# Optimization experiments

Hardware: AMD Instinct MI355X
Metric: run time of the kernel (lower is better)

The kernel has to match this reference:

```python
import jax, jax.numpy as jnp
import numpy as np

B, IN, K, E = 2048, 1024, 128, 64  # batch, in_features, n_concepts, emb_size


def setup_inputs() -> dict:
    key = jax.random.key(0)
    k1, k2, k3, k4, k5 = jax.random.split(key, 5)
    x = jax.random.normal(k1, (B, IN), dtype=jnp.float32)
    # stacked per-concept Linear(in_features, 2*emb_size)
    W = jax.random.normal(k2, (K, IN, 2 * E), dtype=jnp.float32) * (1.0 / np.sqrt(IN))
    b = jax.random.normal(k3, (K, 2 * E), dtype=jnp.float32) * 0.01
    # shared prob predictor Linear(2*emb_size, 1)
    wp = jax.random.normal(k4, (2 * E,), dtype=jnp.float32) * (1.0 / np.sqrt(2 * E))
    bp = jax.random.normal(k5, (), dtype=jnp.float32) * 0.01
    return {"x": x, "W": W, "b": b, "wp": wp, "bp": bp}


def reference(x, W, b, wp, bp):
    # batched GEMM over all concepts at once: [B,K,2E]
    context = jax.nn.leaky_relu(jnp.einsum('bi,kio->bko', x, W) + b)
    # shared predictor + sigmoid: [B,K]
    c_pred = jax.nn.sigmoid(jnp.einsum('bko,o->bk', context, wp) + bp)
    ctx_pos = context[..., :E]
    ctx_neg = context[..., E:]
    p = c_pred[..., None]
    c_emb = ctx_pos * p + ctx_neg * (1.0 - p)  # [B,K,E]
    return c_emb, c_pred
```

## Files before the change

### kernel.cpp

```cpp
#include <hip/hip_runtime.h>

typedef unsigned int u32;
typedef unsigned short u16;
typedef __attribute__((ext_vector_type(8))) __bf16 bf16x8;
typedef __attribute__((ext_vector_type(4))) float f32x4;

#define B_SZ 2048
#define IN_SZ 1024
#define K_SZ 128
#define E_SZ 64
#define TWOE 128
static const size_t OUT_EMB = (size_t)B_SZ * K_SZ * E_SZ;

__device__ __forceinline__ u16 f2bf(float f) {
    u32 u = __builtin_bit_cast(u32, f);
    u32 r = u + 0x7fffu + ((u >> 16) & 1u);
    return (u16)(r >> 16);
}

__device__ __forceinline__ void async16(const void* g, void* l) {
    __builtin_amdgcn_global_load_lds((const __attribute__((address_space(1))) u32*)g,
                                     (__attribute__((address_space(3))) u32*)l, 16, 0, 0);
}

__global__ void __launch_bounds__(256) cvt_x(const float* __restrict__ in, u16* __restrict__ outp, int n4) {
    int i = blockIdx.x * blockDim.x + threadIdx.x;
    if (i < n4) {
        float4 v = ((const float4*)in)[i];
        u32 lo = (u32)f2bf(v.x) | ((u32)f2bf(v.y) << 16);
        u32 hi = (u32)f2bf(v.z) | ((u32)f2bf(v.w) << 16);
        ((uint2*)outp)[i] = make_uint2(lo, hi);
    }
}

__global__ void __launch_bounds__(256) cvt_w(const float* __restrict__ W, u16* __restrict__ wt) {
    __shared__ u16 tr[128][72];
    const int k = blockIdx.y, i0 = blockIdx.x * 64;
    const float* src = W + (size_t)k * IN_SZ * TWOE + (size_t)i0 * TWOE;
#pragma unroll
    for (int r = 0; r < 8; ++r) {
        int idx = r * 256 + threadIdx.x;
        int i = idx >> 5;
        int o = (idx & 31) * 4;
        float4 v = ((const float4*)src)[idx];
        tr[o + 0][i] = f2bf(v.x);
        tr[o + 1][i] = f2bf(v.y);
        tr[o + 2][i] = f2bf(v.z);
        tr[o + 3][i] = f2bf(v.w);
    }
    __syncthreads();
    const int o = threadIdx.x >> 1, h = threadIdx.x & 1;
    u16* dst = wt + ((size_t)(k * TWOE + o) * IN_SZ) + i0 + h * 32;
#pragma unroll
    for (int s = 0; s < 4; ++s) {
        uint4 v = *(const uint4*)&tr[o][h * 32 + s * 8];
        ((uint4*)dst)[s] = v;
    }
}

__global__ void __launch_bounds__(256) cvt_pred(const float* __restrict__ pw, float* __restrict__ out) {
    __shared__ float t[128][132];
    const int b0 = blockIdx.x * 128;
    const int tid = threadIdx.x;
#pragma unroll
    for (int i = 0; i < 16; ++i) {
        int idx = i * 256 + tid;
        int kk = idx >> 5, c4 = (idx & 31) * 4;
        float4 v = *(const float4*)(pw + (size_t)kk * B_SZ + b0 + c4);
        t[kk][c4 + 0] = v.x; t[kk][c4 + 1] = v.y; t[kk][c4 + 2] = v.z; t[kk][c4 + 3] = v.w;
    }
    __syncthreads();
#pragma unroll
    for (int i = 0; i < 16; ++i) {
        int idx = i * 256 + tid;
        int bl = idx >> 5, k4 = (idx & 31) * 4;
        float4 v = make_float4(t[k4 + 0][bl], t[k4 + 1][bl], t[k4 + 2][bl], t[k4 + 3][bl]);
        *(float4*)(out + OUT_EMB + (size_t)(b0 + bl) * K_SZ + k4) = v;
    }
}

__global__ void __launch_bounds__(512, 2) fused_main(
    const u16* __restrict__ xb,
    const u16* __restrict__ wt,
    const float* __restrict__ bias, const float* __restrict__ wpv,
    const float* __restrict__ bpp, float* __restrict__ out,
    float* __restrict__ pw) {
    __shared__ union {
        u16 stage[65536];
        struct { float pl[2][256][2]; float ex[2][256][66]; } epi;
    } sm;
    char* smb = (char*)&sm;

    const int tid = threadIdx.x;
    const int l = tid & 63, w = tid >> 6;
    const int wm = w >> 2, wn = w & 3;
    const int hi = l >> 4, lo16 = l & 15;
    const int q = l >> 2;
    const int swz = (l & 3) ^ ((l >> 3) & 3);

    const int id = blockIdx.x;
    const int xcd = id & 7, j = id >> 3;
    const int kp = (xcd << 3) | (j >> 3);
    const int brow = (j & 7) << 8;

    const u16* abase = xb + (size_t)(brow + w * 16 + q) * IN_SZ + swz * 8;
    const u16* bbase = wt + ((size_t)kp * 256 + w * 16 + q) * IN_SZ + swz * 8;

    const int xsl = (hi ^ ((lo16 >> 1) & 3)) << 4;

    f32x4 acc[8][4] = {};

    auto SA = [&](int d, int kh, int t) {
        u16* dst = (u16*)&sm + (d * 2 + kh) * 8192 + w * 512;
        const u16* src = abase + t * 64 + kh * 32;
        async16(src, dst);
        async16(src + (size_t)128 * IN_SZ, dst + 4096);
    };
    auto SB = [&](int d, int kh, int t) {
        u16* dst = (u16*)&sm + 32768 + (d * 2 + kh) * 8192 + w * 512;
        const u16* src = bbase + t * 64 + kh * 32;
        async16(src, dst);
        async16(src + (size_t)128 * IN_SZ, dst + 4096);
    };

#define NOPX ((void)0)
#define PH(D, KH, STG, VMW)                                                      \
    {                                                                            \
        const char* ra = smb + ((D) * 2 + (KH)) * 16384;                         \
        const char* rb = smb + 65536 + ((D) * 2 + (KH)) * 16384;                 \
        bf16x8 af[8], bfr[4];                                                    \
        _Pragma("unroll") for (int n = 0; n < 4; ++n)                            \
            bfr[n] = *(const bf16x8*)(rb + (wn * 64 + n * 16 + lo16) * 64 + xsl); \
        _Pragma("unroll") for (int mm = 0; mm < 8; ++mm)                         \
            af[mm] = *(const bf16x8*)(ra + (wm * 128 + mm * 16 + lo16) * 64 + xsl); \
        STG;                                                                     \
        __builtin_amdgcn_s_setprio(1);                                           \
        _Pragma("unroll") for (int mm = 0; mm < 8; ++mm)                         \
            _Pragma("unroll") for (int n = 0; n < 4; ++n)                        \
                acc[mm][n] = __builtin_amdgcn_mfma_f32_16x16x32_bf16(            \
                    af[mm], bfr[n], acc[mm][n], 0, 0, 0);                        \
        __builtin_amdgcn_s_setprio(0);                                           \
        asm volatile("s_waitcnt " VMW ::: "memory");                             \
        __builtin_amdgcn_s_barrier();                                            \
    }

    SA(0, 0, 0); SB(0, 0, 0); SA(0, 1, 0); SB(0, 1, 0);
    asm volatile("s_waitcnt vmcnt(4)" ::: "memory");
    __builtin_amdgcn_s_barrier();

#pragma unroll 1
    for (int tt = 0; tt < 14; tt += 2) {
        PH(0, 0, (SA(1, 0, tt + 1), SB(1, 0, tt + 1)), "vmcnt(4)");
        PH(0, 1, (SA(1, 1, tt + 1), SB(1, 1, tt + 1)), "vmcnt(4)");
        PH(1, 0, (SA(0, 0, tt + 2), SB(0, 0, tt + 2)), "vmcnt(4)");
        PH(1, 1, (SA(0, 1, tt + 2), SB(0, 1, tt + 2)), "vmcnt(4)");
    }
    PH(0, 0, (SA(1, 0, 15), SB(1, 0, 15)), "vmcnt(4)");
    PH(0, 1, (SA(1, 1, 15), SB(1, 1, 15)), "vmcnt(4)");
    PH(1, 0, NOPX, "vmcnt(0)");
    PH(1, 1, NOPX, "vmcnt(0)");
#undef PH

    const int ksel = wn >> 1, oh = wn & 1;
    const int kglob = kp * 2 + ksel;
    const float bp_val = *bpp;
    float bvals[4], wvals[4];
#pragma unroll
    for (int n = 0; n < 4; ++n) {
        const int o = oh * 64 + n * 16 + lo16;
        bvals[n] = bias[kglob * TWOE + o];
        wvals[n] = wpv[o];
    }
    float p[8][4];
#pragma unroll
    for (int m = 0; m < 8; ++m)
#pragma unroll
        for (int jj = 0; jj < 4; ++jj) {
            float s = 0.f;
#pragma unroll
            for (int n = 0; n < 4; ++n) {
                float v = acc[m][n][jj] + bvals[n];
                v = v > 0.f ? v : 0.01f * v;
                acc[m][n][jj] = v;
                s += v * wvals[n];
            }
            s += __shfl_xor(s, 1);
            s += __shfl_xor(s, 2);
            s += __shfl_xor(s, 4);
            s += __shfl_xor(s, 8);
            p[m][jj] = s;
        }
    if (lo16 == 0) {
#pragma unroll
        for (int m = 0; m < 8; ++m)
#pragma unroll
            for (int jj = 0; jj < 4; ++jj)
                sm.epi.pl[ksel][wm * 128 + m * 16 + hi * 4 + jj][oh] = p[m][jj];
    }
    __builtin_amdgcn_s_barrier();
#pragma unroll
    for (int m = 0; m < 8; ++m)
#pragma unroll
        for (int jj = 0; jj < 4; ++jj) {
            const int rg = wm * 128 + m * 16 + hi * 4 + jj;
            const float z = sm.epi.pl[ksel][rg][0] + sm.epi.pl[ksel][rg][1] + bp_val;
            p[m][jj] = 1.f / (1.f + __expf(-z));
        }
    if (oh == 0 && lo16 == 0) {
        if (pw) {
#pragma unroll
            for (int m = 0; m < 8; ++m) {
                float4 v = make_float4(p[m][0], p[m][1], p[m][2], p[m][3]);
                *(float4*)(pw + (size_t)kglob * B_SZ + brow + wm * 128 + m * 16 + hi * 4) = v;
            }
        } else {
#pragma unroll
            for (int m = 0; m < 8; ++m)
#pragma unroll
                for (int jj = 0; jj < 4; ++jj) {
                    const int b = brow + wm * 128 + m * 16 + hi * 4 + jj;
                    out[OUT_EMB + (size_t)b * K_SZ + kglob] = p[m][jj];
                }
        }
    }
    if (oh == 1) {
#pragma unroll
        for (int m = 0; m < 8; ++m)
#pragma unroll
            for (int n = 0; n < 4; ++n)
#pragma unroll
                for (int jj = 0; jj < 4; ++jj)
                    sm.epi.ex[ksel][wm * 128 + m * 16 + hi * 4 + jj][n * 16 + lo16] =
                        (1.f - p[m][jj]) * acc[m][n][jj];
    }
    __builtin_amdgcn_s_barrier();
    if (oh == 0) {
#pragma unroll
        for (int m = 0; m < 8; ++m)
#pragma unroll
            for (int n = 0; n < 4; ++n)
#pragma unroll
                for (int jj = 0; jj < 4; ++jj) {
                    const int rl = wm * 128 + m * 16 + hi * 4 + jj;
                    const int b = brow + rl;
                    const int e = n * 16 + lo16;
                    out[((size_t)b * K_SZ + kglob) * E_SZ + e] =
                        p[m][jj] * acc[m][n][jj] + sm.epi.ex[ksel][rl][e];
                }
    }
}

__global__ void __launch_bounds__(128) fallback_kernel(
    const float* __restrict__ x, const float* __restrict__ W,
    const float* __restrict__ bias, const float* __restrict__ wpv,
    const float* __restrict__ bpp, float* __restrict__ out) {
    const int k = blockIdx.y;
    const int b0 = blockIdx.x * 8;
    const int o = threadIdx.x;
    __shared__ float xs[8][1024];
    __shared__ float red[2];
    __shared__ float exch[64];
    for (int idx = threadIdx.x; idx < 8 * 1024; idx += 128)
        xs[idx >> 10][idx & 1023] = x[(size_t)(b0 + (idx >> 10)) * IN_SZ + (idx & 1023)];
    __syncthreads();
    float a[8] = {};
    for (int i = 0; i < 1024; ++i) {
        float wv = W[((size_t)k * IN_SZ + i) * TWOE + o];
#pragma unroll
        for (int bb = 0; bb < 8; ++bb) a[bb] += xs[bb][i] * wv;
    }
    const float bo = bias[k * TWOE + o], wo = wpv[o], bpv = *bpp;
    for (int bb = 0; bb < 8; ++bb) {
        float c = a[bb] + bo;
        c = c > 0.f ? c : 0.01f * c;
        float s = c * wo;
        for (int off = 1; off < 64; off <<= 1) s += __shfl_xor(s, off);
        if ((threadIdx.x & 63) == 0) red[threadIdx.x >> 6] = s;
        __syncthreads();
        float p = 1.f / (1.f + expf(-(red[0] + red[1] + bpv)));
        if (o >= 64) exch[o - 64] = (1.f - p) * c;
        __syncthreads();
        if (o < 64) out[((size_t)(b0 + bb) * K_SZ + k) * E_SZ + o] = p * c + exch[o];
        if (o == 0) out[OUT_EMB + (size_t)(b0 + bb) * K_SZ + k] = p;
        __syncthreads();
    }
}

extern "C" void kernel_launch(void* const* d_in, const int* in_sizes, int n_in,
                              void* d_out, int out_size, void* d_ws, size_t ws_size,
                              hipStream_t stream) {
    const float* x = (const float*)d_in[0];
    const float* W = (const float*)d_in[1];
    const float* bias = (const float*)d_in[2];
    const float* wp = (const float*)d_in[3];
    const float* bp = (const float*)d_in[4];
    float* out = (float*)d_out;

    const size_t X_ELEMS = (size_t)B_SZ * IN_SZ;
    const size_t WT_ELEMS = (size_t)K_SZ * TWOE * IN_SZ;
    const size_t PW_ELEMS = (size_t)K_SZ * B_SZ;
    const size_t NEED_BASE = (X_ELEMS + WT_ELEMS) * sizeof(u16);
    const size_t NEED_FULL = NEED_BASE + PW_ELEMS * sizeof(float);

    if (ws_size >= NEED_BASE) {
        u16* xb = (u16*)d_ws;
        u16* wt = xb + X_ELEMS;
        float* pw = (ws_size >= NEED_FULL) ? (float*)(wt + WT_ELEMS) : nullptr;
        int n4 = (int)(X_ELEMS / 4);
        cvt_x<<<dim3((n4 + 255) / 256), 256, 0, stream>>>(x, xb, n4);
        cvt_w<<<dim3(16, 128), 256, 0, stream>>>(W, wt);
        fused_main<<<dim3(512), 512, 0, stream>>>(xb, wt, bias, wp, bp, out, pw);
        if (pw) cvt_pred<<<dim3(16), 256, 0, stream>>>(pw, out);
    } else {
        fallback_kernel<<<dim3(B_SZ / 8, K_SZ), 128, 0, stream>>>(x, W, bias, wp, bp, out);
    }
}
```

Measured before the change: 114.8 us.

## Restructure GEMM main loop to one barrier per K-tile with staggered half order

Replaces the four-phase macro pipeline, which had a barrier after every half-tile, with a loop that issues all async loads for the next tile up front and then computes both K-halves of the current tile. A single vmcnt(0) wait and barrier closes each tile. The half order is staggered by wm so waves in different rows read different LDS halves first, which should reduce LDS bank contention. The trade-off is fewer syncs against a coarser prefetch depth, since the kernel now waits on all outstanding loads at the end of each tile.

```diff
diff --git a/kernel.cpp b/kernel.cpp
--- a/kernel.cpp
+++ b/kernel.cpp
@@ -123,43 +123,45 @@
         async16(src + (size_t)128 * IN_SZ, dst + 4096);
     };
 
-#define NOPX ((void)0)
-#define PH(D, KH, STG, VMW)                                                      \
-    {                                                                            \
-        const char* ra = smb + ((D) * 2 + (KH)) * 16384;                         \
-        const char* rb = smb + 65536 + ((D) * 2 + (KH)) * 16384;                 \
-        bf16x8 af[8], bfr[4];                                                    \
-        _Pragma("unroll") for (int n = 0; n < 4; ++n)                            \
-            bfr[n] = *(const bf16x8*)(rb + (wn * 64 + n * 16 + lo16) * 64 + xsl); \
-        _Pragma("unroll") for (int mm = 0; mm < 8; ++mm)                         \
-            af[mm] = *(const bf16x8*)(ra + (wm * 128 + mm * 16 + lo16) * 64 + xsl); \
-        STG;                                                                     \
-        __builtin_amdgcn_s_setprio(1);                                           \
-        _Pragma("unroll") for (int mm = 0; mm < 8; ++mm)                         \
-            _Pragma("unroll") for (int n = 0; n < 4; ++n)                        \
-                acc[mm][n] = __builtin_amdgcn_mfma_f32_16x16x32_bf16(            \
-                    af[mm], bfr[n], acc[mm][n], 0, 0, 0);                        \
-        __builtin_amdgcn_s_setprio(0);                                           \
-        asm volatile("s_waitcnt " VMW ::: "memory");                             \
-        __builtin_amdgcn_s_barrier();                                            \
-    }
+    auto PHN = [&](int d, int kh) {
+        const char* ra = smb + (d * 2 + kh) * 16384;
+        const char* rb = smb + 65536 + (d * 2 + kh) * 16384;
+        bf16x8 af[8], bfr[4];
+#pragma unroll
+        for (int n = 0; n < 4; ++n)
+            bfr[n] = *(const bf16x8*)(rb + (wn * 64 + n * 16 + lo16) * 64 + xsl);
+#pragma unroll
+        for (int mm = 0; mm < 8; ++mm)
+            af[mm] = *(const bf16x8*)(ra + (wm * 128 + mm * 16 + lo16) * 64 + xsl);
+        __builtin_amdgcn_s_setprio(1);
+#pragma unroll
+        for (int mm = 0; mm < 8; ++mm)
+#pragma unroll
+            for (int n = 0; n < 4; ++n)
+                acc[mm][n] = __builtin_amdgcn_mfma_f32_16x16x32_bf16(
+                    af[mm], bfr[n], acc[mm][n], 0, 0, 0);
+        __builtin_amdgcn_s_setprio(0);
+    };
+
+    const int khf = wm;
 
     SA(0, 0, 0); SB(0, 0, 0); SA(0, 1, 0); SB(0, 1, 0);
-    asm volatile("s_waitcnt vmcnt(4)" ::: "memory");
+    asm volatile("s_waitcnt vmcnt(0)" ::: "memory");
     __builtin_amdgcn_s_barrier();
 
 #pragma unroll 1
-    for (int tt = 0; tt < 14; tt += 2) {
-        PH(0, 0, (SA(1, 0, tt + 1), SB(1, 0, tt + 1)), "vmcnt(4)");
-        PH(0, 1, (SA(1, 1, tt + 1), SB(1, 1, tt + 1)), "vmcnt(4)");
-        PH(1, 0, (SA(0, 0, tt + 2), SB(0, 0, tt + 2)), "vmcnt(4)");
-        PH(1, 1, (SA(0, 1, tt + 2), SB(0, 1, tt + 2)), "vmcnt(4)");
-    }
-    PH(0, 0, (SA(1, 0, 15), SB(1, 0, 15)), "vmcnt(4)");
-    PH(0, 1, (SA(1, 1, 15), SB(1, 1, 15)), "vmcnt(4)");
-    PH(1, 0, NOPX, "vmcnt(0)");
-    PH(1, 1, NOPX, "vmcnt(0)");
-#undef PH
+    for (int t = 0; t < 16; ++t) {
+        const int d = t & 1, dn = d ^ 1;
+        if (t < 15) {
+            SA(dn, 0, t + 1); SB(dn, 0, t + 1);
+            SA(dn, 1, t + 1); SB(dn, 1, t + 1);
+            asm volatile("" ::: "memory");
+        }
+        PHN(d, khf);
+        PHN(d, khf ^ 1);
+        asm volatile("s_waitcnt vmcnt(0)" ::: "memory");
+        __builtin_amdgcn_s_barrier();
+    }
 
     const int ksel = wn >> 1, oh = wn & 1;
     const int kglob = kp * 2 + ksel;
```

Result: no change. 115.7 us (+0.8%).
